# Kernel tuning notes

Measured on AMD Instinct MI355X. Metric: run time of the kernel, lower is better.

The kernel has to match this reference:

```python
import jax, jax.numpy as jnp
import numpy as np

D = 256        # model_dim
E = 4          # num_experts
H = 8          # attention heads
L = 8          # layers
P = 4          # patch size
IMG = 128
B = 8
NUM_CLASSES = 10
T = (IMG // P) ** 2  # 1024 tokens


def _ln(x, g, b):
    mu = jnp.mean(x, -1, keepdims=True)
    var = jnp.mean((x - mu) ** 2, -1, keepdims=True)
    return (x - mu) * jax.lax.rsqrt(var + 1e-5) * g + b


def setup_inputs() -> dict:
    key = jax.random.key(0)
    ks = jax.random.split(key, 24)
    n = lambda k, s, sc=0.02: jax.random.normal(k, s, jnp.float32) * sc
    return {
        "x": jax.random.normal(ks[0], (B, 3, IMG, IMG), jnp.float32),
        "patch_w": n(ks[1], (D, 3, P, P), 0.1),
        "patch_b": n(ks[2], (D,), 0.01),
        "pos_emb": n(ks[3], (1, T, D), 0.02),
        "router_w": n(ks[4], (E, D), 0.05),
        "router_b": n(ks[5], (E,), 0.01),
        "ln1_g": jnp.ones((L, D), jnp.float32),
        "ln1_b": jnp.zeros((L, D), jnp.float32),
        "q_w": n(ks[6], (L, D, D), 0.05),
        "q_b": n(ks[7], (L, D), 0.01),
        "k_w": n(ks[8], (L, D, D), 0.05),
        "k_b": n(ks[9], (L, D), 0.01),
        "v_w": n(ks[10], (L, D, D), 0.05),
        "v_b": n(ks[11], (L, D), 0.01),
        "o_w": n(ks[12], (L, D, D), 0.05),
        "o_b": n(ks[13], (L, D), 0.01),
        "ln2_g": jnp.ones((L, D), jnp.float32),
        "ln2_b": jnp.zeros((L, D), jnp.float32),
        "l1_w": n(ks[14], (L, 4 * D, D), 0.05),
        "l1_b": n(ks[15], (L, 4 * D), 0.01),
        "l2_w": n(ks[16], (L, D, 4 * D), 0.05),
        "l2_b": n(ks[17], (L, D), 0.01),
        "head_w": n(ks[18], (NUM_CLASSES, D), 0.05),
        "head_b": n(ks[19], (NUM_CLASSES,), 0.01),
        "alpha": jnp.full((1,), 0.5, jnp.float32),
    }


def reference(x, patch_w, patch_b, pos_emb, router_w, router_b, ln1_g, ln1_b,
              q_w, q_b, k_w, k_b, v_w, v_b, o_w, o_b, ln2_g, ln2_b,
              l1_w, l1_b, l2_w, l2_b, head_w, head_b, alpha):
    b = x.shape[0]
    # patch embed: Conv2d(3, D, P, stride=P)
    h = jax.lax.conv_general_dilated(x, patch_w, (P, P), 'VALID',
                                     dimension_numbers=('NCHW', 'OIHW', 'NCHW'))
    h = h + patch_b[None, :, None, None]
    tok = h.reshape(b, D, -1).transpose(0, 2, 1) + pos_emb   # [B,T,D]
    t = tok.shape[1]
    n_per = t // E  # uniform capacity: floor(T * 1/E)
    raw_prob = jax.nn.softmax(tok @ router_w.T + router_b, axis=-1)  # [B,T,E]
    # greedy routing: expert e takes top n_per of remaining tokens, rows zeroed after
    prob = raw_prob
    bidx = jnp.arange(b)[:, None]
    blocks, pblocks = [], []
    for e in range(E):
        _, idx = jax.lax.top_k(prob[:, :, e], n_per)            # [B,n_per]
        blocks.append(jnp.take_along_axis(tok, idx[:, :, None], axis=1))
        pblocks.append(jnp.take_along_axis(raw_prob, idx[:, :, None], axis=1))
        sel = jnp.zeros((b, t), prob.dtype).at[bidx, idx].set(1.0)
        prob = prob * (1.0 - sel)[:, :, None]
    xs = jnp.concatenate(blocks, axis=1)    # [B,T,D] expert-sorted
    rp = jnp.concatenate(pblocks, axis=1)   # [B,T,E]

    widths = [D // 2 ** e for e in range(E)]  # [256,128,64,32]
    scale = D ** -0.5                         # note: model_dim, not head_dim
    dh = D // H
    for l in range(L):
        # ---- nested-expert MHSA ----
        xn = _ln(xs, ln1_g[l], ln1_b[l])
        qs, ks_, vs = [], [], []
        for e in range(E):
            m = widths[e]
            blk = xn[:, e * n_per:(e + 1) * n_per, :m]
            qs.append(blk @ q_w[l][:, :m].T + q_b[l])
            ks_.append(blk @ k_w[l][:, :m].T + k_b[l])
            vs.append(blk @ v_w[l][:, :m].T + v_b[l])
        q = jnp.concatenate(qs, 1).reshape(b, t, H, dh).transpose(0, 2, 1, 3)
        k = jnp.concatenate(ks_, 1).reshape(b, t, H, dh).transpose(0, 2, 1, 3)
        v = jnp.concatenate(vs, 1).reshape(b, t, H, dh).transpose(0, 2, 1, 3)
        attn = jax.nn.softmax(jnp.einsum('bhqd,bhkd->bhqk', q, k) * scale, axis=-1)
        ao = jnp.einsum('bhqk,bhkd->bhqd', attn, v).transpose(0, 2, 1, 3).reshape(b, t, D)
        outs = []
        for e in range(E):
            m = widths[e]
            sl = slice(e * n_per, (e + 1) * n_per)
            o = ao[:, sl, :m] @ o_w[l][:m, :m].T + o_b[l][:m]
            o = jnp.pad(o, ((0, 0), (0, 0), (0, D - m)))
            outs.append(o + xs[:, sl, :])
        xs = jnp.concatenate(outs, 1)
        # ---- nested-expert MLP ----
        xn = _ln(xs, ln2_g[l], ln2_b[l])
        outs = []
        for e in range(E):
            m = widths[e]
            sl = slice(e * n_per, (e + 1) * n_per)
            blk = xn[:, sl, :m]
            inner = jax.nn.gelu(blk @ l1_w[l][:, :m].T + l1_b[l], approximate=False)
            outer = inner @ l2_w[l][:m, :].T + l2_b[l][:m]
            outer = jnp.pad(outer, ((0, 0), (0, 0), (0, D - m)))
            sf = (alpha[0] * rp[:, sl, e] + 1.0)[:, :, None]
            outs.append(xs[:, sl, :] + sf * outer)
        xs = jnp.concatenate(outs, 1)
    # classification head: mean pool + linear
    return jnp.mean(xs, axis=1) @ head_w.T + head_b
```

## Files before the change

kernel.cpp:

```cpp
#include <hip/hip_runtime.h>
#include <math.h>

#define D 256
#define E 4
#define H 8
#define LYR 8
#define IMG 128
#define BB 8
#define NC 10
#define T 1024
#define NPER 256
#define DH 32
#define D4 1024

using bf16x8 = __attribute__((ext_vector_type(8))) __bf16;
using bf16x4 = __attribute__((ext_vector_type(4))) __bf16;
using f32x4  = __attribute__((ext_vector_type(4))) float;

#define MFMA16(a, b, c) __builtin_amdgcn_mfma_f32_16x16x32_bf16((a), (b), (c), 0, 0, 0)

__global__ void cast6(const float* __restrict__ s0, const float* __restrict__ s1,
                      const float* __restrict__ s2, const float* __restrict__ s3,
                      const float* __restrict__ s4, const float* __restrict__ s5,
                      __bf16* __restrict__ d0, __bf16* __restrict__ d1,
                      __bf16* __restrict__ d2, __bf16* __restrict__ d3,
                      __bf16* __restrict__ d4, __bf16* __restrict__ d5) {
    const long A4 = (long)LYR * D * D / 4;
    const long W4 = (long)LYR * D4 * D / 4;
    long i = (long)blockIdx.x * 256 + threadIdx.x;
    const float* s; __bf16* d; long off;
    if (i < 4 * A4) {
        int w = (int)(i / A4); off = i - (long)w * A4;
        s = w == 0 ? s0 : w == 1 ? s1 : w == 2 ? s2 : s3;
        d = w == 0 ? d0 : w == 1 ? d1 : w == 2 ? d2 : d3;
    } else {
        long j = i - 4 * A4;
        int w = (int)(j / W4); off = j - (long)w * W4;
        s = w ? s5 : s4; d = w ? d5 : d4;
    }
    float4 v = ((const float4*)s)[off];
    bf16x4 o;
    o[0] = (__bf16)v.x; o[1] = (__bf16)v.y; o[2] = (__bf16)v.z; o[3] = (__bf16)v.w;
    ((bf16x4*)d)[off] = o;
}

__global__ void patch_embed(const float* __restrict__ x, const float* __restrict__ pw,
                            const float* __restrict__ pb, const float* __restrict__ pos,
                            float* __restrict__ tok) {
    int t = blockIdx.x, b = blockIdx.y, d = threadIdx.x;
    __shared__ float sx[48];
    int ph = t >> 5, pwc = t & 31;
    if (d < 48) {
        int c = d >> 4, ij = d & 15, i = ij >> 2, j = ij & 3;
        sx[d] = x[(((long)b * 3 + c) * IMG + (ph * 4 + i)) * IMG + (pwc * 4 + j)];
    }
    __syncthreads();
    float acc = pb[d];
    #pragma unroll
    for (int kk = 0; kk < 48; ++kk) acc += sx[kk] * pw[d * 48 + kk];
    tok[((long)b * T + t) * D + d] = acc + pos[(long)t * D + d];
}

__global__ void router(const float* __restrict__ tok, const float* __restrict__ rw,
                       const float* __restrict__ rb, float* __restrict__ rawp) {
    int row = blockIdx.x;
    int lane = threadIdx.x;
    const float* tr = tok + (long)row * D;
    float a0 = 0.f, a1 = 0.f, a2 = 0.f, a3 = 0.f;
    for (int c = lane; c < D; c += 64) {
        float xv = tr[c];
        a0 += xv * rw[0 * D + c];
        a1 += xv * rw[1 * D + c];
        a2 += xv * rw[2 * D + c];
        a3 += xv * rw[3 * D + c];
    }
    for (int off = 32; off; off >>= 1) {
        a0 += __shfl_down(a0, off);
        a1 += __shfl_down(a1, off);
        a2 += __shfl_down(a2, off);
        a3 += __shfl_down(a3, off);
    }
    if (lane == 0) {
        float l0 = a0 + rb[0], l1 = a1 + rb[1], l2 = a2 + rb[2], l3 = a3 + rb[3];
        float mx = fmaxf(fmaxf(l0, l1), fmaxf(l2, l3));
        float e0 = __expf(l0 - mx), e1 = __expf(l1 - mx), e2 = __expf(l2 - mx), e3 = __expf(l3 - mx);
        float inv = 1.0f / (e0 + e1 + e2 + e3);
        rawp[(long)row * 4 + 0] = e0 * inv;
        rawp[(long)row * 4 + 1] = e1 * inv;
        rawp[(long)row * 4 + 2] = e2 * inv;
        rawp[(long)row * 4 + 3] = e3 * inv;
    }
}

__global__ __launch_bounds__(1024) void route_topk(const float* __restrict__ rawp,
                                                   int* __restrict__ perm,
                                                   float* __restrict__ rpsel) {
    int b = blockIdx.x, tid = threadIdx.x;
    int lane = tid & 63, wv = tid >> 6;
    __shared__ unsigned hist[256];
    __shared__ unsigned long long ball[16];
    __shared__ int sb_bin, sb_rem;
    bool assigned = false;
    for (int e = 0; e < E; ++e) {
        float v = rawp[((long)b * T + tid) * E + e];
        unsigned key = assigned ? 0u : __float_as_uint(v);
        unsigned prefix = 0;
        int rem = NPER;
        #pragma unroll
        for (int pass = 3; pass >= 0; --pass) {
            int shift = pass * 8;
            if (tid < 256) hist[tid] = 0;
            __syncthreads();
            bool active = (pass == 3) || ((key >> (shift + 8)) == prefix);
            if (active) atomicAdd(&hist[(key >> shift) & 255], 1u);
            __syncthreads();
            if (tid < 64) {
                unsigned c[4], psum = 0;
                #pragma unroll
                for (int u = 0; u < 4; ++u) { c[u] = hist[tid * 4 + u]; psum += c[u]; }
                unsigned suf = psum;
                #pragma unroll
                for (int off = 1; off < 64; off <<= 1) {
                    unsigned o = __shfl_down(suf, off);
                    if (tid + off < 64) suf += o;
                }
                unsigned El = suf - psum;
                if (El < (unsigned)rem && (unsigned)rem <= suf) {
                    unsigned cab = El;
                    #pragma unroll
                    for (int u = 3; u >= 0; --u) {
                        if ((unsigned)rem > cab && (unsigned)rem <= cab + c[u]) {
                            sb_bin = tid * 4 + u;
                            sb_rem = (int)((unsigned)rem - cab);
                        }
                        cab += c[u];
                    }
                }
            }
            __syncthreads();
            prefix = (prefix << 8) | (unsigned)sb_bin;
            rem = sb_rem;
        }
        unsigned t = prefix;
        bool is_tie = (!assigned) && (key == t);
        unsigned long long mbt = __ballot(is_tie);
        if (lane == 0) ball[wv] = mbt;
        __syncthreads();
        int tierank = 0;
        for (int w2 = 0; w2 < wv; ++w2) tierank += __popcll(ball[w2]);
        tierank += __popcll(mbt & ((1ULL << lane) - 1));
        bool sel = (!assigned) && ((key > t) || (is_tie && tierank < rem));
        __syncthreads();
        unsigned long long mbs = __ballot(sel);
        if (lane == 0) ball[wv] = mbs;
        __syncthreads();
        int rank = 0;
        for (int w2 = 0; w2 < wv; ++w2) rank += __popcll(ball[w2]);
        rank += __popcll(mbs & ((1ULL << lane) - 1));
        if (sel) {
            perm[(long)b * T + e * NPER + rank] = tid;
            rpsel[(long)b * T + e * NPER + rank] = v;
            assigned = true;
        }
        __syncthreads();
    }
}

__global__ void gather_tokens(const float* __restrict__ tok, const int* __restrict__ perm,
                              float* __restrict__ xs) {
    int slot = blockIdx.x, b = blockIdx.y, d = threadIdx.x;
    int src = perm[(long)b * T + slot];
    xs[((long)b * T + slot) * D + d] = tok[((long)b * T + src) * D + d];
}

__device__ __forceinline__ void ln_rows32(const float* __restrict__ src,
                                          const float* __restrict__ g,
                                          const float* __restrict__ bta,
                                          __bf16 (*slds)[264], int tid) {
    int sub = tid & 15, rowh = tid >> 4;
    int col0 = sub * 16;
    float gv[16], bv[16];
    #pragma unroll
    for (int u = 0; u < 4; ++u) {
        float4 gg = *(const float4*)&g[col0 + 4 * u];
        float4 bb = *(const float4*)&bta[col0 + 4 * u];
        gv[4*u] = gg.x; gv[4*u+1] = gg.y; gv[4*u+2] = gg.z; gv[4*u+3] = gg.w;
        bv[4*u] = bb.x; bv[4*u+1] = bb.y; bv[4*u+2] = bb.z; bv[4*u+3] = bb.w;
    }
    #pragma unroll
    for (int half = 0; half < 2; ++half) {
        int r = rowh + half * 16;
        const float* rp = src + (long)r * D + col0;
        float v[16];
        #pragma unroll
        for (int u = 0; u < 4; ++u) {
            float4 vv = *(const float4*)&rp[4 * u];
            v[4*u] = vv.x; v[4*u+1] = vv.y; v[4*u+2] = vv.z; v[4*u+3] = vv.w;
        }
        float s = 0.f;
        #pragma unroll
        for (int u = 0; u < 16; ++u) s += v[u];
        #pragma unroll
        for (int mk = 1; mk < 16; mk <<= 1) s += __shfl_xor(s, mk);
        float mu = s * (1.0f / D);
        float s2 = 0.f;
        #pragma unroll
        for (int u = 0; u < 16; ++u) { v[u] -= mu; s2 += v[u] * v[u]; }
        #pragma unroll
        for (int mk = 1; mk < 16; mk <<= 1) s2 += __shfl_xor(s2, mk);
        float rstd = rsqrtf(s2 * (1.0f / D) + 1e-5f);
        bf16x8 o0, o1;
        #pragma unroll
        for (int u = 0; u < 8; ++u) o0[u] = (__bf16)(v[u] * rstd * gv[u] + bv[u]);
        #pragma unroll
        for (int u = 0; u < 8; ++u) o1[u] = (__bf16)(v[8+u] * rstd * gv[8+u] + bv[8+u]);
        *(bf16x8*)&slds[r][col0]     = o0;
        *(bf16x8*)&slds[r][col0 + 8] = o1;
    }
}

__device__ __forceinline__ void gemm_tile(
    const __bf16* __restrict__ A, int lda,
    const __bf16* __restrict__ W, int ldb,
    int K, int lane, f32x4 acc[2][4])
{
    int lr = lane & 15, lk = (lane >> 4) * 8;
    const __bf16* a0 = A + (long)lr * lda + lk;
    const __bf16* a1 = a0 + 16 * lda;
    const __bf16* b0 = W + (long)lr * ldb + lk;
    const __bf16* b1 = b0 + 16 * ldb;
    const __bf16* b2 = b0 + 32 * ldb;
    const __bf16* b3 = b0 + 48 * ldb;
    #pragma unroll 2
    for (int k = 0; k < K; k += 32) {
        bf16x8 av0 = *(const bf16x8*)(a0 + k);
        bf16x8 av1 = *(const bf16x8*)(a1 + k);
        bf16x8 bv0 = *(const bf16x8*)(b0 + k);
        bf16x8 bv1 = *(const bf16x8*)(b1 + k);
        bf16x8 bv2 = *(const bf16x8*)(b2 + k);
        bf16x8 bv3 = *(const bf16x8*)(b3 + k);
        acc[0][0] = MFMA16(av0, bv0, acc[0][0]);
        acc[0][1] = MFMA16(av0, bv1, acc[0][1]);
        acc[0][2] = MFMA16(av0, bv2, acc[0][2]);
        acc[0][3] = MFMA16(av0, bv3, acc[0][3]);
        acc[1][0] = MFMA16(av1, bv0, acc[1][0]);
        acc[1][1] = MFMA16(av1, bv1, acc[1][1]);
        acc[1][2] = MFMA16(av1, bv2, acc[1][2]);
        acc[1][3] = MFMA16(av1, bv3, acc[1][3]);
    }
}

__global__ __launch_bounds__(256) void qkv_ln_gemm(
    const float* __restrict__ xs,
    const __bf16* __restrict__ qwb, const __bf16* __restrict__ kwb, const __bf16* __restrict__ vwb,
    const float* __restrict__ qb, const float* __restrict__ kb, const float* __restrict__ vb,
    const float* __restrict__ g, const float* __restrict__ bta,
    __bf16* __restrict__ Qb, __bf16* __restrict__ Kb, __bf16* __restrict__ Vt)
{
    int tid = threadIdx.x, lane = tid & 63, wid = tid >> 6;
    int tile = blockIdx.x, which = blockIdx.y, b = blockIdx.z;
    int row0 = tile * 32;
    int m = D >> (row0 >> 8);
    __shared__ __bf16 slds[32][264];
    ln_rows32(xs + ((long)b * T + row0) * D, g, bta, slds, tid);
    __syncthreads();
    const __bf16* W = which == 0 ? qwb : which == 1 ? kwb : vwb;
    const float* bias = which == 0 ? qb : which == 1 ? kb : vb;
    int ncol0 = wid * 64;
    const f32x4 vz = {0.f, 0.f, 0.f, 0.f};
    f32x4 acc[2][4];
    #pragma unroll
    for (int i = 0; i < 2; ++i) { acc[i][0]=vz; acc[i][1]=vz; acc[i][2]=vz; acc[i][3]=vz; }
    gemm_tile(&slds[0][0], 264, W + (long)ncol0 * D, D, m, lane, acc);
    int lr = lane & 15, rg = (lane >> 4) * 4;
    #pragma unroll
    for (int i = 0; i < 2; ++i) {
        int row = row0 + i * 16 + rg;
        #pragma unroll
        for (int j = 0; j < 4; ++j) {
            int n = ncol0 + j * 16 + lr;
            float bvs = bias[n];
            if (which == 2) {
                bf16x4 pk;
                #pragma unroll
                for (int r = 0; r < 4; ++r) pk[r] = (__bf16)(acc[i][j][r] + bvs);
                *(bf16x4*)&Vt[((long)b * D + n) * T + row] = pk;
            } else if (which == 0) {
                #pragma unroll
                for (int r = 0; r < 4; ++r)
                    Qb[((long)b * T + row + r) * D + n] = (__bf16)((acc[i][j][r] + bvs) * 0.0625f);
            } else {
                #pragma unroll
                for (int r = 0; r < 4; ++r)
                    Kb[((long)b * T + row + r) * D + n] = (__bf16)(acc[i][j][r] + bvs);
            }
        }
    }
}

__global__ __launch_bounds__(256) void attn_mfma(
    const __bf16* __restrict__ Qb, const __bf16* __restrict__ Kb,
    const __bf16* __restrict__ Vt, __bf16* __restrict__ aob)
{
    int bid = blockIdx.x;
    int bh = (bid & 7) * 8 + ((bid >> 3) & 7);
    int qt = bid >> 6;
    int b = bh >> 3, h = bh & 7;
    int lane = threadIdx.x & 63, wave = threadIdx.x >> 6;
    int lr = lane & 15, g = lane >> 4;
    int q0 = qt * 128 + wave * 32;
    __shared__ __bf16 plds[4][32][72];
    const f32x4 vz = {0.f, 0.f, 0.f, 0.f};
    bf16x8 qf[2];
    qf[0] = *(const bf16x8*)&Qb[((long)b * T + q0 + lr) * D + h * DH + g * 8];
    qf[1] = *(const bf16x8*)&Qb[((long)b * T + q0 + 16 + lr) * D + h * DH + g * 8];
    f32x4 acc[2][2] = {{vz, vz}, {vz, vz}};
    float ls[2] = {0.f, 0.f};
    const __bf16* kbase = Kb + (long)b * T * D + h * DH + g * 8;
    const __bf16* vbase = Vt + ((long)b * D + h * DH) * T;
    for (int kc = 0; kc < T; kc += 64) {
        bf16x8 kf[4];
        #pragma unroll
        for (int j = 0; j < 4; ++j)
            kf[j] = *(const bf16x8*)(kbase + (long)(kc + 16 * j + lr) * D);
        bf16x8 vf[2][2];
        #pragma unroll
        for (int w = 0; w < 2; ++w)
            #pragma unroll
            for (int df = 0; df < 2; ++df)
                vf[w][df] = *(const bf16x8*)(vbase + (long)(df * 16 + lr) * T + kc + 32 * w + 8 * g);
        #pragma unroll
        for (int qi = 0; qi < 2; ++qi) {
            #pragma unroll
            for (int j = 0; j < 4; ++j) {
                f32x4 s = MFMA16(kf[j], qf[qi], vz);
                float p0 = __expf(s[0]), p1 = __expf(s[1]);
                float p2 = __expf(s[2]), p3 = __expf(s[3]);
                ls[qi] += (p0 + p1) + (p2 + p3);
                bf16x4 pk;
                pk[0] = (__bf16)p0; pk[1] = (__bf16)p1;
                pk[2] = (__bf16)p2; pk[3] = (__bf16)p3;
                *(bf16x4*)&plds[wave][qi * 16 + lr][16 * j + 4 * g] = pk;
            }
        }
        #pragma unroll
        for (int qi = 0; qi < 2; ++qi) {
            #pragma unroll
            for (int w = 0; w < 2; ++w) {
                bf16x8 pa = *(const bf16x8*)&plds[wave][qi * 16 + lr][32 * w + 8 * g];
                acc[qi][0] = MFMA16(pa, vf[w][0], acc[qi][0]);
                acc[qi][1] = MFMA16(pa, vf[w][1], acc[qi][1]);
            }
        }
    }
    #pragma unroll
    for (int qi = 0; qi < 2; ++qi) {
        ls[qi] += __shfl_xor(ls[qi], 16);
        ls[qi] += __shfl_xor(ls[qi], 32);
        float inv = 1.0f / ls[qi];
        #pragma unroll
        for (int r = 0; r < 4; ++r) {
            float invr = __shfl(inv, 4 * g + r);
            long obase = ((long)b * T + q0 + qi * 16 + 4 * g + r) * D + h * DH;
            aob[obase + lr]      = (__bf16)(acc[qi][0][r] * invr);
            aob[obase + 16 + lr] = (__bf16)(acc[qi][1][r] * invr);
        }
    }
}

#define GEMM_PROLOGUE \
    int lane = threadIdx.x & 63, wid = threadIdx.x >> 6; \
    int wm = wid >> 1, wn = wid & 1; \
    int b = blockIdx.z >> 2, e = blockIdx.z & 3; \
    int m = D >> e; \
    const f32x4 vz = {0.f, 0.f, 0.f, 0.f}; \
    f32x4 acc[2][4]; \
    _Pragma("unroll") \
    for (int i = 0; i < 2; ++i) { acc[i][0]=vz; acc[i][1]=vz; acc[i][2]=vz; acc[i][3]=vz; }

__global__ __launch_bounds__(256) void oproj_gemm(
    const __bf16* __restrict__ aob, const __bf16* __restrict__ owb,
    const float* __restrict__ ob, float* __restrict__ xs)
{
    GEMM_PROLOGUE
    if ((int)blockIdx.y * 128 >= m) return;
    int ncol0 = blockIdx.y * 128 + wn * 64;
    int row0 = e * NPER + blockIdx.x * 64 + wm * 32;
    gemm_tile(aob + ((long)b * T + row0) * D, D, owb + (long)ncol0 * D, D, m, lane, acc);
    int lr = lane & 15, rg = (lane >> 4) * 4;
    #pragma unroll
    for (int i = 0; i < 2; ++i) {
        int row = row0 + i * 16 + rg;
        #pragma unroll
        for (int j = 0; j < 4; ++j) {
            int n = ncol0 + j * 16 + lr;
            if (n < m) {
                float bv = ob[n];
                #pragma unroll
                for (int r = 0; r < 4; ++r)
                    xs[((long)b * T + row + r) * D + n] += acc[i][j][r] + bv;
            }
        }
    }
}

__global__ __launch_bounds__(256) void mlp1_ln_gemm(
    const float* __restrict__ xs, const __bf16* __restrict__ w1b,
    const float* __restrict__ b1, const float* __restrict__ g, const float* __restrict__ bta,
    __bf16* __restrict__ innerb)
{
    int tid = threadIdx.x, lane = tid & 63, wid = tid >> 6;
    int tile = blockIdx.x, fq = blockIdx.y, b = blockIdx.z;
    int row0 = tile * 32;
    int m = D >> (row0 >> 8);
    __shared__ __bf16 slds[32][264];
    ln_rows32(xs + ((long)b * T + row0) * D, g, bta, slds, tid);
    __syncthreads();
    int ncol0 = fq * 256 + wid * 64;
    const f32x4 vz = {0.f, 0.f, 0.f, 0.f};
    f32x4 acc[2][4];
    #pragma unroll
    for (int i = 0; i < 2; ++i) { acc[i][0]=vz; acc[i][1]=vz; acc[i][2]=vz; acc[i][3]=vz; }
    gemm_tile(&slds[0][0], 264, w1b + (long)ncol0 * D, D, m, lane, acc);
    int lr = lane & 15, rg = (lane >> 4) * 4;
    #pragma unroll
    for (int i = 0; i < 2; ++i) {
        int row = row0 + i * 16 + rg;
        #pragma unroll
        for (int j = 0; j < 4; ++j) {
            int f = ncol0 + j * 16 + lr;
            float bv = b1[f];
            #pragma unroll
            for (int r = 0; r < 4; ++r) {
                float xv = acc[i][j][r] + bv;
                float gl = 0.5f * xv * (1.0f + erff(xv * 0.70710678118654752f));
                innerb[((long)b * T + row + r) * D4 + f] = (__bf16)gl;
            }
        }
    }
}

__global__ __launch_bounds__(256) void mlp2_gemm(
    const __bf16* __restrict__ innerb, const __bf16* __restrict__ w2b,
    const float* __restrict__ b2, const float* __restrict__ rpsel,
    const float* __restrict__ alpha, float* __restrict__ xs)
{
    GEMM_PROLOGUE
    if ((int)blockIdx.y * 128 >= m) return;
    int ncol0 = blockIdx.y * 128 + wn * 64;
    int row0 = e * NPER + blockIdx.x * 64 + wm * 32;
    gemm_tile(innerb + ((long)b * T + row0) * D4, D4, w2b + (long)ncol0 * D4, D4, D4, lane, acc);
    int lr = lane & 15, rg = (lane >> 4) * 4;
    float a0 = alpha[0];
    #pragma unroll
    for (int i = 0; i < 2; ++i) {
        int row = row0 + i * 16 + rg;
        float sf[4];
        #pragma unroll
        for (int r = 0; r < 4; ++r) sf[r] = a0 * rpsel[(long)b * T + row + r] + 1.0f;
        #pragma unroll
        for (int j = 0; j < 4; ++j) {
            int n = ncol0 + j * 16 + lr;
            if (n < m) {
                float bv = b2[n];
                #pragma unroll
                for (int r = 0; r < 4; ++r)
                    xs[((long)b * T + row + r) * D + n] += sf[r] * (acc[i][j][r] + bv);
            }
        }
    }
}

__global__ void head_partial(const float* __restrict__ xs, float* __restrict__ part) {
    int c = blockIdx.x, b = blockIdx.y, d = threadIdx.x;
    const float* p = xs + ((long)b * T + c * 128) * D + d;
    float s = 0.f;
    #pragma unroll 8
    for (int i = 0; i < 128; ++i) s += p[(long)i * D];
    part[((long)b * 8 + c) * D + d] = s;
}

__global__ void head_final(const float* __restrict__ part, const float* __restrict__ hw,
                           const float* __restrict__ hb, float* __restrict__ out) {
    int b = blockIdx.x, d = threadIdx.x;
    __shared__ float smean[D];
    float s = 0.f;
    #pragma unroll
    for (int c = 0; c < 8; ++c) s += part[((long)b * 8 + c) * D + d];
    smean[d] = s * (1.0f / T);
    __syncthreads();
    if (d < NC) {
        float acc = hb[d];
        for (int c = 0; c < D; ++c) acc += smean[c] * hw[d * D + c];
        out[b * NC + d] = acc;
    }
}

extern "C" void kernel_launch(void* const* d_in, const int* in_sizes, int n_in,
                              void* d_out, int out_size, void* d_ws, size_t ws_size,
                              hipStream_t stream) {
    const float* x      = (const float*)d_in[0];
    const float* patchw = (const float*)d_in[1];
    const float* patchb = (const float*)d_in[2];
    const float* pos    = (const float*)d_in[3];
    const float* rw     = (const float*)d_in[4];
    const float* rb     = (const float*)d_in[5];
    const float* ln1g   = (const float*)d_in[6];
    const float* ln1b   = (const float*)d_in[7];
    const float* qw     = (const float*)d_in[8];
    const float* qbi    = (const float*)d_in[9];
    const float* kw     = (const float*)d_in[10];
    const float* kbi    = (const float*)d_in[11];
    const float* vw     = (const float*)d_in[12];
    const float* vbi    = (const float*)d_in[13];
    const float* ow     = (const float*)d_in[14];
    const float* obi    = (const float*)d_in[15];
    const float* ln2g   = (const float*)d_in[16];
    const float* ln2b   = (const float*)d_in[17];
    const float* l1w    = (const float*)d_in[18];
    const float* l1b    = (const float*)d_in[19];
    const float* l2w    = (const float*)d_in[20];
    const float* l2b    = (const float*)d_in[21];
    const float* hw     = (const float*)d_in[22];
    const float* hb     = (const float*)d_in[23];
    const float* alpha  = (const float*)d_in[24];

    char* p = (char*)d_ws;
    auto alloc = [&](size_t bytes) { void* r = (void*)p; p += (bytes + 255) & ~(size_t)255; return r; };
    const long NTD = (long)BB * T * D;

    float*  tok    = (float*)alloc(NTD * 4);
    float*  xs     = (float*)alloc(NTD * 4);
    float*  rawp   = (float*)alloc((long)BB * T * E * 4);
    float*  rpsel  = (float*)alloc((long)BB * T * 4);
    int*    perm   = (int*)alloc((long)BB * T * 4);
    float*  part   = (float*)alloc((long)BB * 8 * D * 4);
    __bf16* Qb     = (__bf16*)alloc(NTD * 2);
    __bf16* Kb     = (__bf16*)alloc(NTD * 2);
    __bf16* Vt     = (__bf16*)alloc(NTD * 2);
    __bf16* aob    = (__bf16*)alloc(NTD * 2);
    __bf16* innerb = (__bf16*)alloc((long)BB * T * D4 * 2);
    __bf16* qwb    = (__bf16*)alloc((long)LYR * D * D * 2);
    __bf16* kwb    = (__bf16*)alloc((long)LYR * D * D * 2);
    __bf16* vwb    = (__bf16*)alloc((long)LYR * D * D * 2);
    __bf16* owb    = (__bf16*)alloc((long)LYR * D * D * 2);
    __bf16* w1b    = (__bf16*)alloc((long)LYR * D4 * D * 2);
    __bf16* w2b    = (__bf16*)alloc((long)LYR * D * D4 * 2);

    cast6<<<6144, 256, 0, stream>>>(qw, kw, vw, ow, l1w, l2w, qwb, kwb, vwb, owb, w1b, w2b);

    patch_embed<<<dim3(T, BB), D, 0, stream>>>(x, patchw, patchb, pos, tok);
    router<<<BB * T, 64, 0, stream>>>(tok, rw, rb, rawp);
    route_topk<<<BB, 1024, 0, stream>>>(rawp, perm, rpsel);
    gather_tokens<<<dim3(T, BB), D, 0, stream>>>(tok, perm, xs);

    for (int l = 0; l < LYR; ++l) {
        qkv_ln_gemm<<<dim3(32, 3, BB), 256, 0, stream>>>(
            xs, qwb + (long)l * D * D, kwb + (long)l * D * D, vwb + (long)l * D * D,
            qbi + l * D, kbi + l * D, vbi + l * D,
            ln1g + l * D, ln1b + l * D, Qb, Kb, Vt);
        attn_mfma<<<dim3(512), 256, 0, stream>>>(Qb, Kb, Vt, aob);
        oproj_gemm<<<dim3(4, 2, BB * E), 256, 0, stream>>>(
            aob, owb + (long)l * D * D, obi + l * D, xs);
        mlp1_ln_gemm<<<dim3(32, 4, BB), 256, 0, stream>>>(
            xs, w1b + (long)l * D4 * D, l1b + (long)l * D4,
            ln2g + l * D, ln2b + l * D, innerb);
        mlp2_gemm<<<dim3(4, 2, BB * E), 256, 0, stream>>>(
            innerb, w2b + (long)l * D * D4, l2b + l * D, rpsel, alpha, xs);
    }

    head_partial<<<dim3(8, BB), 256, 0, stream>>>(xs, part);
    head_final<<<BB, D, 0, stream>>>(part, hw, hb, (float*)d_out);
}
```

Before: 1.036 ms.

## Fuse o-proj, LN2 and both MLP GEMMs into one per-row-tile kernel

Merges the output projection, second layernorm, MLP up-projection with GELU and down-projection into a single kernel working on 16-row tiles. The 1024-wide hidden activation stays in shared memory instead of going through a global buffer, and three launches per layer collapse to one. QKV is restructured to loop over Q/K/V inside one 16-row block, and patch embedding is fused with the router. The trade-off is smaller tiles (16 rows, one row group per wave) with less weight reuse per block, more per-block serial work, and extra shared-memory use that may lower occupancy.

```diff
diff --git a/kernel.cpp b/kernel.cpp
--- a/kernel.cpp
+++ b/kernel.cpp
@@ -44,11 +44,14 @@
     ((bf16x4*)d)[off] = o;
 }
 
-__global__ void patch_embed(const float* __restrict__ x, const float* __restrict__ pw,
-                            const float* __restrict__ pb, const float* __restrict__ pos,
-                            float* __restrict__ tok) {
+__global__ void patch_router(const float* __restrict__ x, const float* __restrict__ pw,
+                             const float* __restrict__ pb, const float* __restrict__ pos,
+                             const float* __restrict__ rw, const float* __restrict__ rb,
+                             float* __restrict__ tok, float* __restrict__ rawp) {
     int t = blockIdx.x, b = blockIdx.y, d = threadIdx.x;
     __shared__ float sx[48];
+    __shared__ float srow[D];
+    __shared__ float slog[4];
     int ph = t >> 5, pwc = t & 31;
     if (d < 48) {
         int c = d >> 4, ij = d & 15, i = ij >> 2, j = ij & 3;
@@ -58,37 +61,26 @@
     float acc = pb[d];
     #pragma unroll
     for (int kk = 0; kk < 48; ++kk) acc += sx[kk] * pw[d * 48 + kk];
-    tok[((long)b * T + t) * D + d] = acc + pos[(long)t * D + d];
-}
-
-__global__ void router(const float* __restrict__ tok, const float* __restrict__ rw,
-                       const float* __restrict__ rb, float* __restrict__ rawp) {
-    int row = blockIdx.x;
-    int lane = threadIdx.x;
-    const float* tr = tok + (long)row * D;
-    float a0 = 0.f, a1 = 0.f, a2 = 0.f, a3 = 0.f;
-    for (int c = lane; c < D; c += 64) {
-        float xv = tr[c];
-        a0 += xv * rw[0 * D + c];
-        a1 += xv * rw[1 * D + c];
-        a2 += xv * rw[2 * D + c];
-        a3 += xv * rw[3 * D + c];
-    }
-    for (int off = 32; off; off >>= 1) {
-        a0 += __shfl_down(a0, off);
-        a1 += __shfl_down(a1, off);
-        a2 += __shfl_down(a2, off);
-        a3 += __shfl_down(a3, off);
-    }
-    if (lane == 0) {
-        float l0 = a0 + rb[0], l1 = a1 + rb[1], l2 = a2 + rb[2], l3 = a3 + rb[3];
+    float val = acc + pos[(long)t * D + d];
+    tok[((long)b * T + t) * D + d] = val;
+    srow[d] = val;
+    __syncthreads();
+    int wv = d >> 6, lane = d & 63;
+    float a = 0.f;
+    for (int c = lane; c < D; c += 64) a += srow[c] * rw[wv * D + c];
+    for (int off = 32; off; off >>= 1) a += __shfl_down(a, off);
+    if (lane == 0) slog[wv] = a + rb[wv];
+    __syncthreads();
+    if (d == 0) {
+        float l0 = slog[0], l1 = slog[1], l2 = slog[2], l3 = slog[3];
         float mx = fmaxf(fmaxf(l0, l1), fmaxf(l2, l3));
         float e0 = __expf(l0 - mx), e1 = __expf(l1 - mx), e2 = __expf(l2 - mx), e3 = __expf(l3 - mx);
         float inv = 1.0f / (e0 + e1 + e2 + e3);
-        rawp[(long)row * 4 + 0] = e0 * inv;
-        rawp[(long)row * 4 + 1] = e1 * inv;
-        rawp[(long)row * 4 + 2] = e2 * inv;
-        rawp[(long)row * 4 + 3] = e3 * inv;
+        long row = (long)b * T + t;
+        rawp[row * 4 + 0] = e0 * inv;
+        rawp[row * 4 + 1] = e1 * inv;
+        rawp[row * 4 + 2] = e2 * inv;
+        rawp[row * 4 + 3] = e3 * inv;
     }
 }
 
@@ -173,80 +165,72 @@
     xs[((long)b * T + slot) * D + d] = tok[((long)b * T + src) * D + d];
 }
 
-__device__ __forceinline__ void ln_rows32(const float* __restrict__ src,
+__device__ __forceinline__ void ln_rows16(const float* __restrict__ src,
                                           const float* __restrict__ g,
                                           const float* __restrict__ bta,
                                           __bf16 (*slds)[264], int tid) {
-    int sub = tid & 15, rowh = tid >> 4;
+    int sub = tid & 15, r = tid >> 4;
     int col0 = sub * 16;
-    float gv[16], bv[16];
+    float v[16], gv[16], bv[16];
+    const float* rp = src + (long)r * D + col0;
     #pragma unroll
     for (int u = 0; u < 4; ++u) {
+        float4 vv = *(const float4*)&rp[4 * u];
         float4 gg = *(const float4*)&g[col0 + 4 * u];
         float4 bb = *(const float4*)&bta[col0 + 4 * u];
+        v[4*u] = vv.x; v[4*u+1] = vv.y; v[4*u+2] = vv.z; v[4*u+3] = vv.w;
         gv[4*u] = gg.x; gv[4*u+1] = gg.y; gv[4*u+2] = gg.z; gv[4*u+3] = gg.w;
         bv[4*u] = bb.x; bv[4*u+1] = bb.y; bv[4*u+2] = bb.z; bv[4*u+3] = bb.w;
     }
-    #pragma unroll
-    for (int half = 0; half < 2; ++half) {
-        int r = rowh + half * 16;
-        const float* rp = src + (long)r * D + col0;
-        float v[16];
-        #pragma unroll
-        for (int u = 0; u < 4; ++u) {
-            float4 vv = *(const float4*)&rp[4 * u];
-            v[4*u] = vv.x; v[4*u+1] = vv.y; v[4*u+2] = vv.z; v[4*u+3] = vv.w;
-        }
-        float s = 0.f;
-        #pragma unroll
-        for (int u = 0; u < 16; ++u) s += v[u];
-        #pragma unroll
-        for (int mk = 1; mk < 16; mk <<= 1) s += __shfl_xor(s, mk);
-        float mu = s * (1.0f / D);
-        float s2 = 0.f;
-        #pragma unroll
-        for (int u = 0; u < 16; ++u) { v[u] -= mu; s2 += v[u] * v[u]; }
-        #pragma unroll
-        for (int mk = 1; mk < 16; mk <<= 1) s2 += __shfl_xor(s2, mk);
-        float rstd = rsqrtf(s2 * (1.0f / D) + 1e-5f);
-        bf16x8 o0, o1;
-        #pragma unroll
-        for (int u = 0; u < 8; ++u) o0[u] = (__bf16)(v[u] * rstd * gv[u] + bv[u]);
-        #pragma unroll
-        for (int u = 0; u < 8; ++u) o1[u] = (__bf16)(v[8+u] * rstd * gv[8+u] + bv[8+u]);
-        *(bf16x8*)&slds[r][col0]     = o0;
-        *(bf16x8*)&slds[r][col0 + 8] = o1;
-    }
-}
-
+    float s = 0.f;
+    #pragma unroll
+    for (int u = 0; u < 16; ++u) s += v[u];
+    #pragma unroll
+    for (int mk = 1; mk < 16; mk <<= 1) s += __shfl_xor(s, mk);
+    float mu = s * (1.0f / D);
+    float s2 = 0.f;
+    #pragma unroll
+    for (int u = 0; u < 16; ++u) { v[u] -= mu; s2 += v[u] * v[u]; }
+    #pragma unroll
+    for (int mk = 1; mk < 16; mk <<= 1) s2 += __shfl_xor(s2, mk);
+    float rstd = rsqrtf(s2 * (1.0f / D) + 1e-5f);
+    bf16x8 o0, o1;
+    #pragma unroll
+    for (int u = 0; u < 8; ++u) o0[u] = (__bf16)(v[u] * rstd * gv[u] + bv[u]);
+    #pragma unroll
+    for (int u = 0; u < 8; ++u) o1[u] = (__bf16)(v[8+u] * rstd * gv[8+u] + bv[8+u]);
+    *(bf16x8*)&slds[r][col0]     = o0;
+    *(bf16x8*)&slds[r][col0 + 8] = o1;
+}
+
+template<int RG>
 __device__ __forceinline__ void gemm_tile(
     const __bf16* __restrict__ A, int lda,
     const __bf16* __restrict__ W, int ldb,
-    int K, int lane, f32x4 acc[2][4])
+    int K, int lane, f32x4 (&acc)[RG][4])
 {
     int lr = lane & 15, lk = (lane >> 4) * 8;
     const __bf16* a0 = A + (long)lr * lda + lk;
-    const __bf16* a1 = a0 + 16 * lda;
     const __bf16* b0 = W + (long)lr * ldb + lk;
     const __bf16* b1 = b0 + 16 * ldb;
     const __bf16* b2 = b0 + 32 * ldb;
     const __bf16* b3 = b0 + 48 * ldb;
     #pragma unroll 2
     for (int k = 0; k < K; k += 32) {
-        bf16x8 av0 = *(const bf16x8*)(a0 + k);
-        bf16x8 av1 = *(const bf16x8*)(a1 + k);
+        bf16x8 av[RG];
+        #pragma unroll
+        for (int i = 0; i < RG; ++i) av[i] = *(const bf16x8*)(a0 + i * 16 * lda + k);
         bf16x8 bv0 = *(const bf16x8*)(b0 + k);
         bf16x8 bv1 = *(const bf16x8*)(b1 + k);
         bf16x8 bv2 = *(const bf16x8*)(b2 + k);
         bf16x8 bv3 = *(const bf16x8*)(b3 + k);
-        acc[0][0] = MFMA16(av0, bv0, acc[0][0]);
-        acc[0][1] = MFMA16(av0, bv1, acc[0][1]);
-        acc[0][2] = MFMA16(av0, bv2, acc[0][2]);
-        acc[0][3] = MFMA16(av0, bv3, acc[0][3]);
-        acc[1][0] = MFMA16(av1, bv0, acc[1][0]);
-        acc[1][1] = MFMA16(av1, bv1, acc[1][1]);
-        acc[1][2] = MFMA16(av1, bv2, acc[1][2]);
-        acc[1][3] = MFMA16(av1, bv3, acc[1][3]);
+        #pragma unroll
+        for (int i = 0; i < RG; ++i) {
+            acc[i][0] = MFMA16(av[i], bv0, acc[i][0]);
+            acc[i][1] = MFMA16(av[i], bv1, acc[i][1]);
+            acc[i][2] = MFMA16(av[i], bv2, acc[i][2]);
+            acc[i][3] = MFMA16(av[i], bv3, acc[i][3]);
+        }
     }
 }
 
@@ -258,41 +242,39 @@
     __bf16* __restrict__ Qb, __bf16* __restrict__ Kb, __bf16* __restrict__ Vt)
 {
     int tid = threadIdx.x, lane = tid & 63, wid = tid >> 6;
-    int tile = blockIdx.x, which = blockIdx.y, b = blockIdx.z;
-    int row0 = tile * 32;
+    int tile = blockIdx.x, b = blockIdx.y;
+    int row0 = tile * 16;
     int m = D >> (row0 >> 8);
-    __shared__ __bf16 slds[32][264];
-    ln_rows32(xs + ((long)b * T + row0) * D, g, bta, slds, tid);
-    __syncthreads();
-    const __bf16* W = which == 0 ? qwb : which == 1 ? kwb : vwb;
-    const float* bias = which == 0 ? qb : which == 1 ? kb : vb;
+    __shared__ __bf16 slds[16][264];
+    ln_rows16(xs + ((long)b * T + row0) * D, g, bta, slds, tid);
+    __syncthreads();
     int ncol0 = wid * 64;
+    int lr = lane & 15, rg = (lane >> 4) * 4;
     const f32x4 vz = {0.f, 0.f, 0.f, 0.f};
-    f32x4 acc[2][4];
-    #pragma unroll
-    for (int i = 0; i < 2; ++i) { acc[i][0]=vz; acc[i][1]=vz; acc[i][2]=vz; acc[i][3]=vz; }
-    gemm_tile(&slds[0][0], 264, W + (long)ncol0 * D, D, m, lane, acc);
-    int lr = lane & 15, rg = (lane >> 4) * 4;
-    #pragma unroll
-    for (int i = 0; i < 2; ++i) {
-        int row = row0 + i * 16 + rg;
+    #pragma unroll
+    for (int which = 0; which < 3; ++which) {
+        const __bf16* W = which == 0 ? qwb : which == 1 ? kwb : vwb;
+        const float* bias = which == 0 ? qb : which == 1 ? kb : vb;
+        f32x4 acc[1][4] = {{vz, vz, vz, vz}};
+        gemm_tile<1>(&slds[0][0], 264, W + (long)ncol0 * D, D, m, lane, acc);
         #pragma unroll
         for (int j = 0; j < 4; ++j) {
             int n = ncol0 + j * 16 + lr;
             float bvs = bias[n];
+            int row = row0 + rg;
             if (which == 2) {
                 bf16x4 pk;
                 #pragma unroll
-                for (int r = 0; r < 4; ++r) pk[r] = (__bf16)(acc[i][j][r] + bvs);
+                for (int r = 0; r < 4; ++r) pk[r] = (__bf16)(acc[0][j][r] + bvs);
                 *(bf16x4*)&Vt[((long)b * D + n) * T + row] = pk;
             } else if (which == 0) {
                 #pragma unroll
                 for (int r = 0; r < 4; ++r)
-                    Qb[((long)b * T + row + r) * D + n] = (__bf16)((acc[i][j][r] + bvs) * 0.0625f);
+                    Qb[((long)b * T + row + r) * D + n] = (__bf16)((acc[0][j][r] + bvs) * 0.0625f);
             } else {
                 #pragma unroll
                 for (int r = 0; r < 4; ++r)
-                    Kb[((long)b * T + row + r) * D + n] = (__bf16)(acc[i][j][r] + bvs);
+                    Kb[((long)b * T + row + r) * D + n] = (__bf16)(acc[0][j][r] + bvs);
             }
         }
     }
@@ -368,29 +350,27 @@
     }
 }
 
-#define GEMM_PROLOGUE \
-    int lane = threadIdx.x & 63, wid = threadIdx.x >> 6; \
-    int wm = wid >> 1, wn = wid & 1; \
-    int b = blockIdx.z >> 2, e = blockIdx.z & 3; \
-    int m = D >> e; \
-    const f32x4 vz = {0.f, 0.f, 0.f, 0.f}; \
-    f32x4 acc[2][4]; \
-    _Pragma("unroll") \
-    for (int i = 0; i < 2; ++i) { acc[i][0]=vz; acc[i][1]=vz; acc[i][2]=vz; acc[i][3]=vz; }
-
-__global__ __launch_bounds__(256) void oproj_gemm(
+__global__ __launch_bounds__(256) void oproj_mlp(
     const __bf16* __restrict__ aob, const __bf16* __restrict__ owb,
-    const float* __restrict__ ob, float* __restrict__ xs)
+    const float* __restrict__ ob,
+    const float* __restrict__ g2, const float* __restrict__ b2g,
+    const __bf16* __restrict__ w1b, const float* __restrict__ b1,
+    const __bf16* __restrict__ w2b, const float* __restrict__ b2,
+    const float* __restrict__ rpsel, const float* __restrict__ alpha,
+    float* __restrict__ xs)
 {
-    GEMM_PROLOGUE
-    if ((int)blockIdx.y * 128 >= m) return;
-    int ncol0 = blockIdx.y * 128 + wn * 64;
-    int row0 = e * NPER + blockIdx.x * 64 + wm * 32;
-    gemm_tile(aob + ((long)b * T + row0) * D, D, owb + (long)ncol0 * D, D, m, lane, acc);
+    int tid = threadIdx.x, lane = tid & 63, wid = tid >> 6;
+    int tile = blockIdx.x, b = blockIdx.y;
+    int row0 = tile * 16;
+    int m = D >> (row0 >> 8);
+    __shared__ __bf16 slds[16][264];
+    __shared__ __bf16 inner[16][520];
     int lr = lane & 15, rg = (lane >> 4) * 4;
-    #pragma unroll
-    for (int i = 0; i < 2; ++i) {
-        int row = row0 + i * 16 + rg;
+    int ncol0 = wid * 64;
+    const f32x4 vz = {0.f, 0.f, 0.f, 0.f};
+    if (ncol0 < m) {
+        f32x4 acc[1][4] = {{vz, vz, vz, vz}};
+        gemm_tile<1>(aob + ((long)b * T + row0) * D, D, owb + (long)ncol0 * D, D, m, lane, acc);
         #pragma unroll
         for (int j = 0; j < 4; ++j) {
             int n = ncol0 + j * 16 + lr;
@@ -398,66 +378,43 @@
                 float bv = ob[n];
                 #pragma unroll
                 for (int r = 0; r < 4; ++r)
-                    xs[((long)b * T + row + r) * D + n] += acc[i][j][r] + bv;
-            }
-        }
-    }
-}
-
-__global__ __launch_bounds__(256) void mlp1_ln_gemm(
-    const float* __restrict__ xs, const __bf16* __restrict__ w1b,
-    const float* __restrict__ b1, const float* __restrict__ g, const float* __restrict__ bta,
-    __bf16* __restrict__ innerb)
-{
-    int tid = threadIdx.x, lane = tid & 63, wid = tid >> 6;
-    int tile = blockIdx.x, fq = blockIdx.y, b = blockIdx.z;
-    int row0 = tile * 32;
-    int m = D >> (row0 >> 8);
-    __shared__ __bf16 slds[32][264];
-    ln_rows32(xs + ((long)b * T + row0) * D, g, bta, slds, tid);
-    __syncthreads();
-    int ncol0 = fq * 256 + wid * 64;
-    const f32x4 vz = {0.f, 0.f, 0.f, 0.f};
-    f32x4 acc[2][4];
-    #pragma unroll
-    for (int i = 0; i < 2; ++i) { acc[i][0]=vz; acc[i][1]=vz; acc[i][2]=vz; acc[i][3]=vz; }
-    gemm_tile(&slds[0][0], 264, w1b + (long)ncol0 * D, D, m, lane, acc);
-    int lr = lane & 15, rg = (lane >> 4) * 4;
-    #pragma unroll
-    for (int i = 0; i < 2; ++i) {
-        int row = row0 + i * 16 + rg;
-        #pragma unroll
-        for (int j = 0; j < 4; ++j) {
-            int f = ncol0 + j * 16 + lr;
-            float bv = b1[f];
+                    xs[((long)b * T + row0 + rg + r) * D + n] += acc[0][j][r] + bv;
+            }
+        }
+    }
+    __syncthreads();
+    ln_rows16(xs + ((long)b * T + row0) * D, g2, b2g, slds, tid);
+    __syncthreads();
+    f32x4 acc2[1][4] = {{vz, vz, vz, vz}};
+    #pragma unroll
+    for (int c = 0; c < 2; ++c) {
+        #pragma unroll
+        for (int half = 0; half < 2; ++half) {
+            int f0 = c * 512 + wid * 128 + half * 64;
+            f32x4 a1[1][4] = {{vz, vz, vz, vz}};
+            gemm_tile<1>(&slds[0][0], 264, w1b + (long)f0 * D, D, m, lane, a1);
             #pragma unroll
-            for (int r = 0; r < 4; ++r) {
-                float xv = acc[i][j][r] + bv;
-                float gl = 0.5f * xv * (1.0f + erff(xv * 0.70710678118654752f));
-                innerb[((long)b * T + row + r) * D4 + f] = (__bf16)gl;
-            }
-        }
-    }
-}
-
-__global__ __launch_bounds__(256) void mlp2_gemm(
-    const __bf16* __restrict__ innerb, const __bf16* __restrict__ w2b,
-    const float* __restrict__ b2, const float* __restrict__ rpsel,
-    const float* __restrict__ alpha, float* __restrict__ xs)
-{
-    GEMM_PROLOGUE
-    if ((int)blockIdx.y * 128 >= m) return;
-    int ncol0 = blockIdx.y * 128 + wn * 64;
-    int row0 = e * NPER + blockIdx.x * 64 + wm * 32;
-    gemm_tile(innerb + ((long)b * T + row0) * D4, D4, w2b + (long)ncol0 * D4, D4, D4, lane, acc);
-    int lr = lane & 15, rg = (lane >> 4) * 4;
-    float a0 = alpha[0];
-    #pragma unroll
-    for (int i = 0; i < 2; ++i) {
-        int row = row0 + i * 16 + rg;
+            for (int j = 0; j < 4; ++j) {
+                int f = f0 + j * 16 + lr;
+                float bv = b1[f];
+                int fl = f - c * 512;
+                #pragma unroll
+                for (int r = 0; r < 4; ++r) {
+                    float xv = a1[0][j][r] + bv;
+                    inner[rg + r][fl] = (__bf16)(0.5f * xv * (1.0f + erff(xv * 0.70710678118654752f)));
+                }
+            }
+        }
+        __syncthreads();
+        if (ncol0 < m)
+            gemm_tile<1>(&inner[0][0], 520, w2b + (long)ncol0 * D4 + c * 512, D4, 512, lane, acc2);
+        __syncthreads();
+    }
+    if (ncol0 < m) {
+        float a0 = alpha[0];
         float sf[4];
         #pragma unroll
-        for (int r = 0; r < 4; ++r) sf[r] = a0 * rpsel[(long)b * T + row + r] + 1.0f;
+        for (int r = 0; r < 4; ++r) sf[r] = a0 * rpsel[(long)b * T + row0 + rg + r] + 1.0f;
         #pragma unroll
         for (int j = 0; j < 4; ++j) {
             int n = ncol0 + j * 16 + lr;
@@ -465,7 +422,7 @@
                 float bv = b2[n];
                 #pragma unroll
                 for (int r = 0; r < 4; ++r)
-                    xs[((long)b * T + row + r) * D + n] += sf[r] * (acc[i][j][r] + bv);
+                    xs[((long)b * T + row0 + rg + r) * D + n] += sf[r] * (acc2[0][j][r] + bv);
             }
         }
     }
@@ -539,7 +496,6 @@
     __bf16* Kb     = (__bf16*)alloc(NTD * 2);
     __bf16* Vt     = (__bf16*)alloc(NTD * 2);
     __bf16* aob    = (__bf16*)alloc(NTD * 2);
-    __bf16* innerb = (__bf16*)alloc((long)BB * T * D4 * 2);
     __bf16* qwb    = (__bf16*)alloc((long)LYR * D * D * 2);
     __bf16* kwb    = (__bf16*)alloc((long)LYR * D * D * 2);
     __bf16* vwb    = (__bf16*)alloc((long)LYR * D * D * 2);
@@ -549,24 +505,22 @@
 
     cast6<<<6144, 256, 0, stream>>>(qw, kw, vw, ow, l1w, l2w, qwb, kwb, vwb, owb, w1b, w2b);
 
-    patch_embed<<<dim3(T, BB), D, 0, stream>>>(x, patchw, patchb, pos, tok);
-    router<<<BB * T, 64, 0, stream>>>(tok, rw, rb, rawp);
+    patch_router<<<dim3(T, BB), 256, 0, stream>>>(x, patchw, patchb, pos, rw, rb, tok, rawp);
     route_topk<<<BB, 1024, 0, stream>>>(rawp, perm, rpsel);
-    gather_tokens<<<dim3(T, BB), D, 0, stream>>>(tok, perm, xs);
+    gather_tokens<<<dim3(T, BB), 256, 0, stream>>>(tok, perm, xs);
 
     for (int l = 0; l < LYR; ++l) {
-        qkv_ln_gemm<<<dim3(32, 3, BB), 256, 0, stream>>>(
+        qkv_ln_gemm<<<dim3(64, BB), 256, 0, stream>>>(
             xs, qwb + (long)l * D * D, kwb + (long)l * D * D, vwb + (long)l * D * D,
             qbi + l * D, kbi + l * D, vbi + l * D,
             ln1g + l * D, ln1b + l * D, Qb, Kb, Vt);
         attn_mfma<<<dim3(512), 256, 0, stream>>>(Qb, Kb, Vt, aob);
-        oproj_gemm<<<dim3(4, 2, BB * E), 256, 0, stream>>>(
-            aob, owb + (long)l * D * D, obi + l * D, xs);
-        mlp1_ln_gemm<<<dim3(32, 4, BB), 256, 0, stream>>>(
-            xs, w1b + (long)l * D4 * D, l1b + (long)l * D4,
-            ln2g + l * D, ln2b + l * D, innerb);
-        mlp2_gemm<<<dim3(4, 2, BB * E), 256, 0, stream>>>(
-            innerb, w2b + (long)l * D * D4, l2b + l * D, rpsel, alpha, xs);
+        oproj_mlp<<<dim3(64, BB), 256, 0, stream>>>(
+            aob, owb + (long)l * D * D, obi + l * D,
+            ln2g + l * D, ln2b + l * D,
+            w1b + (long)l * D4 * D, l1b + (long)l * D4,
+            w2b + (long)l * D * D4, l2b + l * D,
+            rpsel, alpha, xs);
     }
 
     head_partial<<<dim3(8, BB), 256, 0, stream>>>(xs, part);
```

Result: slower. 1.194 ms (+15.3%).
